# Kernel optimization log

Measured on AMD Instinct MI355X. Metric: run time of the kernel, lower is better.

Reference implementation:

```python
import jax, jax.numpy as jnp
import numpy as np

EPS = 1e-5
KS = 3  # deformable kernel size
K2 = KS * KS


def conv2d(x, w, stride=1, padding=1):
    return jax.lax.conv_general_dilated(
        x, w, window_strides=(stride, stride),
        padding=[(padding, padding), (padding, padding)],
        dimension_numbers=("NCHW", "OIHW", "NCHW"))


def batchnorm(x, gamma, beta):
    # training-mode BN: batch statistics over (N, H, W)
    mean = jnp.mean(x, axis=(0, 2, 3), keepdims=True)
    var = jnp.var(x, axis=(0, 2, 3), keepdims=True)
    xhat = (x - mean) * jax.lax.rsqrt(var + EPS)
    return xhat * gamma[None, :, None, None] + beta[None, :, None, None]


def deform_conv(x, offsets, w, pad=1):
    # x: (B,C,H,W); offsets: (B,2*K2,H,W) -> first K2 channels = row (y)
    # offsets, next K2 = col (x) offsets; w: (O,C,KS,KS)
    B, C, H, W = x.shape
    xp = jnp.pad(x, ((0, 0), (0, 0), (pad, pad), (pad, pad)))
    Hp, Wp = H + 2 * pad, W + 2 * pad
    # base grid (center of each output pixel in padded coords)
    p0_y = jnp.arange(H, dtype=x.dtype) + pad            # (H,)
    p0_x = jnp.arange(W, dtype=x.dtype) + pad            # (W,)
    # kernel tap offsets in [-1, 0, 1]^2, row-major
    pn = jnp.stack(jnp.meshgrid(jnp.arange(KS) - pad, jnp.arange(KS) - pad,
                                indexing="ij"), axis=-1).reshape(K2, 2).astype(x.dtype)
    off = offsets.reshape(B, 2, K2, H, W)
    off_y = jnp.transpose(off[:, 0], (0, 2, 3, 1))       # (B,H,W,K2)
    off_x = jnp.transpose(off[:, 1], (0, 2, 3, 1))
    py = p0_y[None, :, None, None] + pn[:, 0][None, None, None, :] + off_y
    px = p0_x[None, None, :, None] + pn[:, 1][None, None, None, :] + off_x
    py = jnp.clip(py, 0.0, Hp - 1.0)
    px = jnp.clip(px, 0.0, Wp - 1.0)
    y0 = jnp.floor(py).astype(jnp.int32)
    x0 = jnp.floor(px).astype(jnp.int32)
    y1 = jnp.minimum(y0 + 1, Hp - 1)
    x1 = jnp.minimum(x0 + 1, Wp - 1)
    wy = (py - y0.astype(x.dtype))[:, None]              # (B,1,H,W,K2)
    wx = (px - x0.astype(x.dtype))[:, None]

    def gather(xb, yi, xi):                              # xb (C,Hp,Wp)
        return xb[:, yi, xi]                             # (C,H,W,K2)
    g = jax.vmap(gather)
    v00 = g(xp, y0, x0)
    v01 = g(xp, y0, x1)
    v10 = g(xp, y1, x0)
    v11 = g(xp, y1, x1)
    sampled = (v00 * (1 - wy) * (1 - wx) + v01 * (1 - wy) * wx +
               v10 * wy * (1 - wx) + v11 * wy * wx)      # (B,C,H,W,K2)
    return jnp.einsum("bchwk,ock->bohw", sampled, w.reshape(w.shape[0], C, K2))


def setup_inputs() -> dict:
    key = jax.random.key(0)
    ks = jax.random.split(key, 16)
    B, Cin, P, H, W = 64, 64, 64, 64, 64
    s = lambda k, shp, fan: jax.random.normal(k, shp, jnp.float32) * (fan ** -0.5)
    return {
        "x": jax.random.normal(ks[0], (B, Cin, H, W), jnp.float32),
        "conv1_w": s(ks[1], (P, Cin, 3, 3), Cin * 9),
        "bn1_g": jnp.ones((P,), jnp.float32), "bn1_b": jnp.zeros((P,), jnp.float32),
        "conv2_w": s(ks[2], (16, P, 1, 1), P),
        "bn2_g": jnp.ones((16,), jnp.float32), "bn2_b": jnp.zeros((16,), jnp.float32),
        "off_w": s(ks[3], (18, 16, 3, 3), 16 * 9) * 0.1,
        "off_b": jnp.zeros((18,), jnp.float32),
        "conv3_w": s(ks[4], (16, 16, 3, 3), 16 * 9),
        "bn3_g": jnp.ones((16,), jnp.float32), "bn3_b": jnp.zeros((16,), jnp.float32),
        "conv4_w": s(ks[5], (P, 16, 3, 3), 16 * 9),
        "bn4_g": jnp.ones((P,), jnp.float32), "bn4_b": jnp.zeros((P,), jnp.float32),
    }


def reference(x, conv1_w, bn1_g, bn1_b, conv2_w, bn2_g, bn2_b, off_w, off_b,
              conv3_w, bn3_g, bn3_b, conv4_w, bn4_g, bn4_b):
    out = jax.nn.relu(batchnorm(conv2d(x, conv1_w, 1, 1), bn1_g, bn1_b))
    out = jax.nn.relu(batchnorm(conv2d(out, conv2_w, 1, 0), bn2_g, bn2_b))
    offsets = conv2d(out, off_w, 1, 1) + off_b[None, :, None, None]
    out = jax.nn.relu(batchnorm(deform_conv(out, offsets, conv3_w), bn3_g, bn3_b))
    out = batchnorm(conv2d(out, conv4_w, 1, 1), bn4_g, bn4_b)
    out = out + x  # identity shortcut (stride=1, in_planes==planes)
    return jax.nn.relu(out)
```

## Files before the change

kernel.cpp:

```cpp
#include <hip/hip_runtime.h>

#define BN_N 262144.0f

typedef unsigned short u16;
typedef __attribute__((ext_vector_type(8))) short short8;
typedef __attribute__((ext_vector_type(4))) float floatx4;

#define RP1 4224
#define IS1 278784
#define RP2 1584
#define IS2 104544
#define H2P_TOTAL 6690816

static __device__ __forceinline__ u16 f2bf(float f) {
  union { float f; unsigned u; } v; v.f = f;
  unsigned u = v.u;
  return (u16)((u + 0x7FFFu + ((u >> 16) & 1u)) >> 16);
}
static __device__ __forceinline__ float bf2f(u16 h) {
  union { unsigned u; float f; } v; v.u = ((unsigned)h) << 16;
  return v.f;
}
static __device__ __forceinline__ void cp16(const u16* g, u16* l) {
  __builtin_amdgcn_global_load_lds((const __attribute__((address_space(1))) unsigned int*)g,
                                   (__attribute__((address_space(3))) unsigned int*)l, 16, 0, 0);
}

__global__ __launch_bounds__(256) void prep_weights_k(const float* __restrict__ w1,
                                                      const float* __restrict__ w4,
                                                      const float* __restrict__ w3,
                                                      const float* __restrict__ ow,
                                                      u16* __restrict__ Bsw, u16* __restrict__ Bsw4,
                                                      u16* __restrict__ Bsw3, u16* __restrict__ BswO) {
  int blk = blockIdx.x, tid = threadIdx.x;
  if (blk < 144) {
    int d = blk * 256 + tid;
    int kin = d & 7, n = (d >> 3) & 63, kgrp = (d >> 9) & 3, kc = d >> 11;
    int k = kc * 32 + kgrp * 8 + kin;
    int tap = k >> 6, c = k & 63;
    Bsw[d] = f2bf(w1[n * 576 + c * 9 + tap]);
  } else if (blk < 184) {
    int d = (blk - 144) * 256 + tid;
    int kin = d & 7, n = (d >> 3) & 63, lkk = (d >> 9) & 3, kk = d >> 11;
    int tap = kk * 2 + (lkk >> 1);
    int c = ((lkk & 1) << 3) + kin;
    float v = (tap < 9) ? w4[n * 144 + c * 9 + tap] : 0.f;
    Bsw4[d] = f2bf(v);
  } else if (blk < 194) {
    int d = (blk - 184) * 256 + tid;
    int kin = d & 7, n = (d >> 3) & 15, lkk = (d >> 7) & 3, kk = d >> 9;
    int k = kk * 32 + lkk * 8 + kin;
    int tap = k >> 4, c = k & 15;
    float v = (tap < 9) ? w3[n * 144 + c * 9 + tap] : 0.f;
    Bsw3[d] = f2bf(v);
  } else {
    int d = (blk - 194) * 256 + tid;
    int kin = d & 7, n = (d >> 3) & 31, lkk = (d >> 8) & 3, kk = d >> 10;
    int tap = kk * 2 + (lkk >> 1);
    int c = ((lkk & 1) << 3) + kin;
    float v = (tap < 9 && n < 18) ? ow[n * 144 + c * 9 + tap] : 0.f;
    BswO[d] = f2bf(v);
  }
}

__global__ __launch_bounds__(256) void prep_x_k(const float* __restrict__ x,
                                                u16* __restrict__ xp) {
  int yp = blockIdx.x;
  int b = blockIdx.y;
  int tid = threadIdx.x;
  u16* rowbase = xp + (size_t)(b * 66 + yp) * RP1;
  if (yp == 0 || yp == 65) {
    for (int i = tid; i < RP1 / 4; i += 256)
      ((ushort4*)rowbase)[i] = make_ushort4(0, 0, 0, 0);
    return;
  }
  int y = yp - 1;
  __shared__ __align__(16) u16 s[64][72];
  for (int i = tid; i < 4096; i += 256) {
    int c = i >> 6, xx = i & 63;
    s[xx][c] = f2bf(x[((b * 64 + c) << 12) + (y << 6) + xx]);
  }
  if (tid < 128) {
    int c = tid & 63;
    int pxp = (tid >> 6) ? 65 : 0;
    rowbase[pxp * 64 + c] = 0;
  }
  __syncthreads();
  for (int j = tid; j < 512; j += 256) {
    int xx = j >> 3, chunk = j & 7;
    int pxp = xx + 1;
    int ph = chunk ^ (pxp & 7);
    *(short8*)(rowbase + pxp * 64 + ph * 8) = *(const short8*)(&s[xx][chunk * 8]);
  }
}

__global__ __launch_bounds__(512, 2) void conv1_mfma(const u16* __restrict__ xp,
                                                     const u16* __restrict__ Bsw,
                                                     u16* __restrict__ h1,
                                                     float* __restrict__ sum1, float* __restrict__ sq1) {
  __shared__ __align__(16) u16 ring[43520];
  __shared__ float LS[256], LQ[256];
  const int tid = threadIdx.x;
  const int w8 = tid >> 6, l = tid & 63;
  const int r = w8 & 3, g = w8 >> 2;
  const int lm = l & 15, lk = l >> 4;
  const int b = blockIdx.x >> 2;
  const int quarter = blockIdx.x & 3;
  const int c0 = quarter * 8;
  const u16* xb = xp + (size_t)b * 66 * RP1;

  short8 bReg[18][2];
#pragma unroll
  for (int kk = 0; kk < 18; ++kk)
#pragma unroll
    for (int j = 0; j < 2; ++j)
      bReg[kk][j] = *(const short8*)(Bsw + (((kk * 4 + lk) * 64) + (g * 2 + j) * 16 + lm) * 8);

#pragma unroll
  for (int c = 0; c < 3; ++c) {
    const u16* src = xb + (size_t)(2 * (c0 + c)) * RP1;
    u16* dst = ring + ((c0 + c) % 5) * 8704;
    for (int s = w8; s < 17; s += 8) cp16(src + s * 512 + l * 8, dst + s * 512);
  }
  asm volatile("s_waitcnt vmcnt(0)" ::: "memory");
  __builtin_amdgcn_s_barrier();
  __builtin_amdgcn_sched_barrier(0);

  float ssum[2] = {0.f, 0.f}, sqsm[2] = {0.f, 0.f};

#pragma unroll 1
  for (int j = 0; j < 4; ++j) {
    const int y0 = quarter * 16 + j * 4;
    if (j < 3) {
#pragma unroll
      for (int c = 0; c < 2; ++c) {
        const int ch = c0 + 2 * j + 3 + c;
        const u16* src = xb + (size_t)(2 * ch) * RP1;
        u16* dst = ring + (ch % 5) * 8704;
        for (int s = w8; s < 17; s += 8) cp16(src + s * 512 + l * 8, dst + s * 512);
      }
      __builtin_amdgcn_sched_barrier(0);
    }

    floatx4 acc[4][2];
#pragma unroll
    for (int mt = 0; mt < 4; ++mt)
#pragma unroll
      for (int nb = 0; nb < 2; ++nb)
        acc[mt][nb] = (floatx4){0.f, 0.f, 0.f, 0.f};

#pragma unroll
    for (int kk = 0; kk < 18; ++kk) {
      const int tap = kk >> 1;
      const int dy = (tap < 3) ? 0 : ((tap < 6) ? 1 : 2);
      const int dx = tap - dy * 3;
      const int chunk16 = ((kk & 1) << 2) + lk;
      const int pr = y0 + r + dy;
      const u16* abase = ring + ((pr >> 1) % 5) * 8704 + (pr & 1) * 4224;
      short8 aF[4];
#pragma unroll
      for (int mt = 0; mt < 4; ++mt) {
        int pxp = mt * 16 + lm + dx;
        int ph = chunk16 ^ (pxp & 7);
        aF[mt] = *(const short8*)(abase + pxp * 64 + ph * 8);
      }
#pragma unroll
      for (int mt = 0; mt < 4; ++mt)
#pragma unroll
        for (int nb = 0; nb < 2; ++nb)
          acc[mt][nb] = __builtin_amdgcn_mfma_f32_16x16x32_bf16(aF[mt], bReg[kk][nb], acc[mt][nb], 0, 0, 0);
    }

    const int y = y0 + r;
#pragma unroll
    for (int mt = 0; mt < 4; ++mt)
#pragma unroll
      for (int nb = 0; nb < 2; ++nb) {
        const int oc = g * 32 + nb * 16 + lm;
        u16* dst = h1 + ((size_t)(b * 64 + oc) << 12) + (y << 6) + mt * 16 + (lk << 2);
        floatx4 v = acc[mt][nb];
        *(ushort4*)dst = make_ushort4(f2bf(v.x), f2bf(v.y), f2bf(v.z), f2bf(v.w));
      }

#pragma unroll
    for (int nb = 0; nb < 2; ++nb)
#pragma unroll
      for (int mt = 0; mt < 4; ++mt) {
        floatx4 a = acc[mt][nb];
        ssum[nb] += a.x + a.y + a.z + a.w;
        sqsm[nb] += a.x * a.x + a.y * a.y + a.z * a.z + a.w * a.w;
      }

    if (j < 3) {
      asm volatile("s_waitcnt vmcnt(8)" ::: "memory");
      __builtin_amdgcn_s_barrier();
      __builtin_amdgcn_sched_barrier(0);
    }
  }

#pragma unroll
  for (int nb = 0; nb < 2; ++nb) {
    ssum[nb] += __shfl_xor(ssum[nb], 16, 64);  ssum[nb] += __shfl_xor(ssum[nb], 32, 64);
    sqsm[nb] += __shfl_xor(sqsm[nb], 16, 64);  sqsm[nb] += __shfl_xor(sqsm[nb], 32, 64);
  }
  if (lk == 0) {
#pragma unroll
    for (int nb = 0; nb < 2; ++nb) {
      const int oc = g * 32 + nb * 16 + lm;
      LS[r * 64 + oc] = ssum[nb];  LQ[r * 64 + oc] = sqsm[nb];
    }
  }
  __syncthreads();
  if (tid < 64) atomicAdd(&sum1[tid], LS[tid] + LS[64 + tid] + LS[128 + tid] + LS[192 + tid]);
  else if (tid < 128) { int o = tid - 64; atomicAdd(&sq1[o], LQ[o] + LQ[64 + o] + LQ[128 + o] + LQ[192 + o]); }
}

__global__ __launch_bounds__(256) void conv2_k(const u16* __restrict__ h1,
                                               const float* __restrict__ w2,
                                               const float* __restrict__ sum1, const float* __restrict__ sq1,
                                               const float* __restrict__ g1, const float* __restrict__ b1,
                                               u16* __restrict__ out,
                                               float* __restrict__ sum2, float* __restrict__ sq2) {
  __shared__ float s_wt[64 * 16];
  __shared__ float s_scale[64], s_shift[64];
  __shared__ float ls[4][16], lsq[4][16];
  int tid = threadIdx.x;
  for (int i = tid; i < 1024; i += 256) {
    int o = i >> 6, c = i & 63;
    s_wt[c * 16 + o] = w2[i];
  }
  if (tid < 64) {
    float m = sum1[tid] / BN_N;
    float var = sq1[tid] / BN_N - m * m;
    float sc = g1[tid] * rsqrtf(var + 1e-5f);
    s_scale[tid] = sc;
    s_shift[tid] = b1[tid] - m * sc;
  }
  __syncthreads();
  int p = blockIdx.x * 256 + tid;
  int b = p >> 12, r = p & 4095;
  const u16* src = h1 + ((size_t)b << 18) + r;
  float acc[16];
#pragma unroll
  for (int o = 0; o < 16; ++o) acc[o] = 0.f;
  for (int c = 0; c < 64; ++c) {
    float v = bf2f(src[c << 12]);
    v = fmaxf(v * s_scale[c] + s_shift[c], 0.f);
    const float* wp = &s_wt[c * 16];
    float4 w0 = *(const float4*)wp;
    float4 w1 = *(const float4*)(wp + 4);
    float4 w2v = *(const float4*)(wp + 8);
    float4 w3v = *(const float4*)(wp + 12);
    acc[0] += w0.x * v;  acc[1] += w0.y * v;  acc[2] += w0.z * v;  acc[3] += w0.w * v;
    acc[4] += w1.x * v;  acc[5] += w1.y * v;  acc[6] += w1.z * v;  acc[7] += w1.w * v;
    acc[8] += w2v.x * v; acc[9] += w2v.y * v; acc[10] += w2v.z * v; acc[11] += w2v.w * v;
    acc[12] += w3v.x * v; acc[13] += w3v.y * v; acc[14] += w3v.z * v; acc[15] += w3v.w * v;
  }
  u16* dst = out + (size_t)p * 16;
  short8 o0, o1;
#pragma unroll
  for (int j = 0; j < 8; ++j) {
    o0[j] = (short)f2bf(acc[j]);
    o1[j] = (short)f2bf(acc[8 + j]);
  }
  *(short8*)(dst) = o0;
  *(short8*)(dst + 8) = o1;
  int lane = tid & 63, wv = tid >> 6;
#pragma unroll
  for (int o = 0; o < 16; ++o) {
    float s = acc[o], s2 = acc[o] * acc[o];
#pragma unroll
    for (int off = 32; off > 0; off >>= 1) {
      s += __shfl_down(s, off, 64);
      s2 += __shfl_down(s2, off, 64);
    }
    if (lane == 0) { ls[wv][o] = s; lsq[wv][o] = s2; }
  }
  __syncthreads();
  if (tid < 16) atomicAdd(&sum2[tid], ls[0][tid] + ls[1][tid] + ls[2][tid] + ls[3][tid]);
  else if (tid < 32) {
    int o = tid - 16;
    atomicAdd(&sq2[o], lsq[0][o] + lsq[1][o] + lsq[2][o] + lsq[3][o]);
  }
}

__global__ __launch_bounds__(256) void bnrelu2_k(const u16* __restrict__ ws2,
                                                 const float* __restrict__ sum2, const float* __restrict__ sq2,
                                                 const float* __restrict__ g2, const float* __restrict__ b2,
                                                 u16* __restrict__ h2p) {
  __shared__ float s_scale[16], s_shift[16];
  int tid = threadIdx.x;
  if (tid < 16) {
    float m = sum2[tid] / BN_N;
    float var = sq2[tid] / BN_N - m * m;
    float sc = g2[tid] * rsqrtf(var + 1e-5f);
    s_scale[tid] = sc;
    s_shift[tid] = b2[tid] - m * sc;
  }
  __syncthreads();
  int p = blockIdx.x * 256 + tid;
  int b = p >> 12, r = p & 4095;
  int y = r >> 6, xx = r & 63;
  const u16* src = ws2 + (size_t)p * 16;
  short8 v0 = *(const short8*)(src);
  short8 v1 = *(const short8*)(src + 8);
  u16* dst = h2p + (size_t)(b * 66 + y + 1) * RP2 + (xx + 1) * 24;
  short8 o0, o1;
#pragma unroll
  for (int j = 0; j < 8; ++j) {
    o0[j] = (short)f2bf(fmaxf(bf2f((u16)v0[j]) * s_scale[j] + s_shift[j], 0.f));
    o1[j] = (short)f2bf(fmaxf(bf2f((u16)v1[j]) * s_scale[j + 8] + s_shift[j + 8], 0.f));
  }
  *(short8*)(dst) = o0;
  *(short8*)(dst + 8) = o1;
}

__global__ __launch_bounds__(256) void offdeform_mfma(const u16* __restrict__ h2p,
                                                      const u16* __restrict__ BswO,
                                                      const float* __restrict__ ob,
                                                      const u16* __restrict__ Bsw3,
                                                      u16* __restrict__ out,
                                                      float* __restrict__ sum3, float* __restrict__ sq3) {
  __shared__ __align__(16) u16 lA[9728];
  __shared__ __align__(16) u16 lB[5120];
  __shared__ float offsT[4][64][20];
  __shared__ float ls[4][16], lsq[4][16];
  const int tid = threadIdx.x;
  const int w = tid >> 6, l = tid & 63;
  const int lm = l & 15, lk = l >> 4;
  const int b = blockIdx.x >> 4;
  const int y0 = (blockIdx.x & 15) << 2;
  const int y = y0 + w;
  const u16* src = h2p + ((size_t)b * 66 + y0) * RP2;
  for (int seg = w; seg < 19; seg += 4) cp16(src + seg * 512 + l * 8, lA + seg * 512);
  for (int seg = w; seg < 10; seg += 4) cp16(BswO + seg * 512 + l * 8, lB + seg * 512);
  __syncthreads();

  floatx4 acc[4][2];
#pragma unroll
  for (int mt = 0; mt < 4; ++mt)
#pragma unroll
    for (int nb = 0; nb < 2; ++nb)
      acc[mt][nb] = (floatx4){0.f, 0.f, 0.f, 0.f};

#pragma unroll
  for (int kk = 0; kk < 5; ++kk) {
    int tap = kk * 2 + (lk >> 1);
    if (tap > 8) tap = 8;
    const int dy = tap / 3, dx = tap - dy * 3;
    const int c0 = (lk & 1) << 3;
    const int rowoff = (w + dy) * RP2;
    short8 aF[4], bF[2];
#pragma unroll
    for (int mt = 0; mt < 4; ++mt)
      aF[mt] = *(const short8*)(lA + rowoff + (mt * 16 + lm + dx) * 24 + c0);
    const u16* bp = lB + (((kk * 4 + lk) * 32) + lm) * 8;
    bF[0] = *(const short8*)(bp);
    bF[1] = *(const short8*)(bp + 128);
#pragma unroll
    for (int mt = 0; mt < 4; ++mt)
#pragma unroll
      for (int nb = 0; nb < 2; ++nb)
        acc[mt][nb] = __builtin_amdgcn_mfma_f32_16x16x32_bf16(aF[mt], bF[nb], acc[mt][nb], 0, 0, 0);
  }

#pragma unroll
  for (int mt = 0; mt < 4; ++mt)
#pragma unroll
    for (int nb = 0; nb < 2; ++nb) {
      int oc = nb * 16 + lm;
      if (oc < 18) {
        float bias = ob[oc];
        floatx4 v = acc[mt][nb];
#pragma unroll
        for (int reg = 0; reg < 4; ++reg)
          offsT[w][mt * 16 + lk * 4 + reg][oc] = v[reg] + bias;
      }
    }
  __syncthreads();

  const u16* img = h2p + (size_t)b * IS2;
  short8 bf[5];
#pragma unroll
  for (int kk = 0; kk < 5; ++kk)
    bf[kk] = *(const short8*)(Bsw3 + (((kk * 4 + lk) * 16) + lm) * 8);

  floatx4 accd[4];
#pragma unroll
  for (int mt = 0; mt < 4; ++mt) accd[mt] = (floatx4){0.f, 0.f, 0.f, 0.f};

#pragma unroll
  for (int mt = 0; mt < 4; ++mt) {
    const int x = mt * 16 + lm;
#pragma unroll
    for (int kk = 0; kk < 5; ++kk) {
      const int k0 = kk * 32 + lk * 8;
      int tap = k0 >> 4;
      const int c0 = k0 & 15;
      if (tap > 8) tap = 8;
      const int dy = tap / 3, dx = tap - dy * 3;
      float offy = offsT[w][x][tap];
      float offx = offsT[w][x][tap + 9];
      float py = (float)(y + dy) + offy;
      float px = (float)(x + dx) + offx;
      py = fminf(fmaxf(py, 0.f), 65.f);
      px = fminf(fmaxf(px, 0.f), 65.f);
      float y0f = floorf(py), x0f = floorf(px);
      int yy0 = (int)y0f, xx0 = (int)x0f;
      int yy1 = min(yy0 + 1, 65), xx1 = min(xx0 + 1, 65);
      float wy = py - y0f, wx = px - x0f;
      float w00 = (1.f - wy) * (1.f - wx), w01 = (1.f - wy) * wx;
      float w10 = wy * (1.f - wx),         w11 = wy * wx;
      short8 v00 = *(const short8*)(img + (yy0 * 66 + xx0) * 24 + c0);
      short8 v01 = *(const short8*)(img + (yy0 * 66 + xx1) * 24 + c0);
      short8 v10 = *(const short8*)(img + (yy1 * 66 + xx0) * 24 + c0);
      short8 v11 = *(const short8*)(img + (yy1 * 66 + xx1) * 24 + c0);
      short8 a;
#pragma unroll
      for (int jj = 0; jj < 8; ++jj) {
        float s = bf2f((u16)v00[jj]) * w00 + bf2f((u16)v01[jj]) * w01
                + bf2f((u16)v10[jj]) * w10 + bf2f((u16)v11[jj]) * w11;
        a[jj] = (short)f2bf(s);
      }
      accd[mt] = __builtin_amdgcn_mfma_f32_16x16x32_bf16(a, bf[kk], accd[mt], 0, 0, 0);
    }
  }

  const int pbase = (b << 12) + (y << 6);
  float s = 0.f, s2 = 0.f;
#pragma unroll
  for (int mt = 0; mt < 4; ++mt) {
    floatx4 a = accd[mt];
    s += a.x + a.y + a.z + a.w;
    s2 += a.x * a.x + a.y * a.y + a.z * a.z + a.w * a.w;
#pragma unroll
    for (int reg = 0; reg < 4; ++reg) {
      int pp = pbase + mt * 16 + lk * 4 + reg;
      out[(size_t)pp * 16 + lm] = f2bf(a[reg]);
    }
  }
  s += __shfl_xor(s, 16, 64);  s += __shfl_xor(s, 32, 64);
  s2 += __shfl_xor(s2, 16, 64); s2 += __shfl_xor(s2, 32, 64);
  if (lk == 0) { ls[w][lm] = s; lsq[w][lm] = s2; }
  __syncthreads();
  if (tid < 16) atomicAdd(&sum3[tid], ls[0][tid] + ls[1][tid] + ls[2][tid] + ls[3][tid]);
  else if (tid < 32) {
    int o = tid - 16;
    atomicAdd(&sq3[o], lsq[0][o] + lsq[1][o] + lsq[2][o] + lsq[3][o]);
  }
}

__global__ __launch_bounds__(256) void bnrelu3_k(const u16* __restrict__ wsd,
                                                 const float* __restrict__ sum3, const float* __restrict__ sq3,
                                                 const float* __restrict__ g3, const float* __restrict__ b3,
                                                 u16* __restrict__ h3p) {
  __shared__ float s_scale[16], s_shift[16];
  int tid = threadIdx.x;
  if (tid < 16) {
    float m = sum3[tid] / BN_N;
    float var = sq3[tid] / BN_N - m * m;
    float sc = g3[tid] * rsqrtf(var + 1e-5f);
    s_scale[tid] = sc;
    s_shift[tid] = b3[tid] - m * sc;
  }
  __syncthreads();
  int p = blockIdx.x * 256 + tid;
  int b = p >> 12, r = p & 4095;
  int y = r >> 6, xx = r & 63;
  const u16* src = wsd + (size_t)p * 16;
  short8 v0 = *(const short8*)(src);
  short8 v1 = *(const short8*)(src + 8);
  u16* dst = h3p + (size_t)(b * 66 + y + 1) * RP2 + (xx + 1) * 24;
  short8 o0, o1;
#pragma unroll
  for (int j = 0; j < 8; ++j) {
    o0[j] = (short)f2bf(fmaxf(bf2f((u16)v0[j]) * s_scale[j] + s_shift[j], 0.f));
    o1[j] = (short)f2bf(fmaxf(bf2f((u16)v1[j]) * s_scale[j + 8] + s_shift[j + 8], 0.f));
  }
  *(short8*)(dst) = o0;
  *(short8*)(dst + 8) = o1;
}

__global__ __launch_bounds__(256) void conv4_mfma(const u16* __restrict__ h3p,
                                                  const u16* __restrict__ Bsw4,
                                                  u16* __restrict__ h4,
                                                  float* __restrict__ sum4, float* __restrict__ sq4) {
  __shared__ __align__(16) u16 lA[9728];
  __shared__ __align__(16) u16 lB[10240];
  const int tid = threadIdx.x;
  const int w = tid >> 6, l = tid & 63;
  const int lm = l & 15, lk = l >> 4;
  const int b = blockIdx.x >> 4;
  const int y0 = (blockIdx.x & 15) << 2;
  const int y = y0 + w;
  const u16* src = h3p + ((size_t)b * 66 + y0) * RP2;
  for (int seg = w; seg < 19; seg += 4) cp16(src + seg * 512 + l * 8, lA + seg * 512);
  for (int seg = w; seg < 20; seg += 4) cp16(Bsw4 + seg * 512 + l * 8, lB + seg * 512);
  __syncthreads();

  floatx4 acc[4][4];
#pragma unroll
  for (int mt = 0; mt < 4; ++mt)
#pragma unroll
    for (int nb = 0; nb < 4; ++nb)
      acc[mt][nb] = (floatx4){0.f, 0.f, 0.f, 0.f};

#pragma unroll
  for (int kk = 0; kk < 5; ++kk) {
    int tap = kk * 2 + (lk >> 1);
    if (tap > 8) tap = 8;
    const int dy = tap / 3, dx = tap - dy * 3;
    const int c0 = (lk & 1) << 3;
    const int rowoff = (w + dy) * RP2;
    short8 aF[4], bF[4];
#pragma unroll
    for (int mt = 0; mt < 4; ++mt)
      aF[mt] = *(const short8*)(lA + rowoff + (mt * 16 + lm + dx) * 24 + c0);
    const u16* bp = lB + (((kk * 4 + lk) * 64) + lm) * 8;
    bF[0] = *(const short8*)(bp);
    bF[1] = *(const short8*)(bp + 128);
    bF[2] = *(const short8*)(bp + 256);
    bF[3] = *(const short8*)(bp + 384);
#pragma unroll
    for (int mt = 0; mt < 4; ++mt)
#pragma unroll
      for (int nb = 0; nb < 4; ++nb)
        acc[mt][nb] = __builtin_amdgcn_mfma_f32_16x16x32_bf16(aF[mt], bF[nb], acc[mt][nb], 0, 0, 0);
  }

#pragma unroll
  for (int mt = 0; mt < 4; ++mt)
#pragma unroll
    for (int nb = 0; nb < 4; ++nb) {
      u16* dst = h4 + ((size_t)(b * 64 + nb * 16 + lm) << 12) + (y << 6) + mt * 16 + (lk << 2);
      floatx4 v = acc[mt][nb];
      *(ushort4*)dst = make_ushort4(f2bf(v.x), f2bf(v.y), f2bf(v.z), f2bf(v.w));
    }

  __syncthreads();
  float* LS = (float*)lA;
  float* LQ = LS + 256;
  float s[4], s2[4];
#pragma unroll
  for (int nb = 0; nb < 4; ++nb) {
    s[nb] = 0.f; s2[nb] = 0.f;
#pragma unroll
    for (int mt = 0; mt < 4; ++mt) {
      floatx4 a = acc[mt][nb];
      s[nb] += a.x + a.y + a.z + a.w;
      s2[nb] += a.x * a.x + a.y * a.y + a.z * a.z + a.w * a.w;
    }
    s[nb] += __shfl_xor(s[nb], 16, 64);  s[nb] += __shfl_xor(s[nb], 32, 64);
    s2[nb] += __shfl_xor(s2[nb], 16, 64); s2[nb] += __shfl_xor(s2[nb], 32, 64);
  }
  if (lk == 0) {
#pragma unroll
    for (int nb = 0; nb < 4; ++nb) { LS[w * 64 + nb * 16 + lm] = s[nb]; LQ[w * 64 + nb * 16 + lm] = s2[nb]; }
  }
  __syncthreads();
  if (tid < 64) atomicAdd(&sum4[tid], LS[tid] + LS[64 + tid] + LS[128 + tid] + LS[192 + tid]);
  else if (tid < 128) { int o = tid - 64; atomicAdd(&sq4[o], LQ[o] + LQ[64 + o] + LQ[128 + o] + LQ[192 + o]); }
}

__global__ __launch_bounds__(256) void final_k(const u16* __restrict__ h4,
                                               float* __restrict__ out,
                                               const float* __restrict__ x,
                                               const float* __restrict__ sum4, const float* __restrict__ sq4,
                                               const float* __restrict__ g4, const float* __restrict__ b4) {
  __shared__ float s_scale[64], s_shift[64];
  int tid = threadIdx.x;
  if (tid < 64) {
    float m = sum4[tid] / BN_N;
    float var = sq4[tid] / BN_N - m * m;
    float sc = g4[tid] * rsqrtf(var + 1e-5f);
    s_scale[tid] = sc;
    s_shift[tid] = b4[tid] - m * sc;
  }
  __syncthreads();
  int i = (blockIdx.x * 256 + tid) * 4;
  int c = (i >> 12) & 63;
  ushort4 q = *(const ushort4*)(h4 + i);
  float4 xv = *(const float4*)(x + i);
  float sc = s_scale[c], sh = s_shift[c];
  float4 v;
  v.x = fmaxf(bf2f(q.x) * sc + sh + xv.x, 0.f);
  v.y = fmaxf(bf2f(q.y) * sc + sh + xv.y, 0.f);
  v.z = fmaxf(bf2f(q.z) * sc + sh + xv.z, 0.f);
  v.w = fmaxf(bf2f(q.w) * sc + sh + xv.w, 0.f);
  *(float4*)(out + i) = v;
}

extern "C" void kernel_launch(void* const* d_in, const int* in_sizes, int n_in,
                              void* d_out, int out_size, void* d_ws, size_t ws_size,
                              hipStream_t stream) {
  const float* x  = (const float*)d_in[0];
  const float* w1 = (const float*)d_in[1];
  const float* g1 = (const float*)d_in[2];
  const float* b1 = (const float*)d_in[3];
  const float* w2 = (const float*)d_in[4];
  const float* g2 = (const float*)d_in[5];
  const float* b2 = (const float*)d_in[6];
  const float* ow = (const float*)d_in[7];
  const float* ob = (const float*)d_in[8];
  const float* w3 = (const float*)d_in[9];
  const float* g3 = (const float*)d_in[10];
  const float* b3 = (const float*)d_in[11];
  const float* w4 = (const float*)d_in[12];
  const float* g4 = (const float*)d_in[13];
  const float* b4 = (const float*)d_in[14];
  float* out = (float*)d_out;
  float* ws = (float*)d_ws;

  float* reg0 = ws;
  float* wsd  = reg0 + 4718592;
  float* ws2  = wsd + 4194304;
  float* h2pf = ws2 + 4194304;
  float* stats = h2pf + 4460544;
  float* sum1 = stats, *sq1 = stats + 64;
  float* sum2 = stats + 128, *sq2 = stats + 144;
  float* sum3 = stats + 160, *sq3 = stats + 176;
  float* sum4 = stats + 192, *sq4 = stats + 256;
  u16* xp   = (u16*)ws;
  u16* Bsw  = (u16*)(stats + 320);
  u16* Bsw4 = Bsw + 36864;
  u16* Bsw3 = Bsw4 + 10240;
  u16* BswO = Bsw3 + 2560;
  u16* h2p  = (u16*)h2pf;
  u16* h4   = (u16*)reg0;
  u16* h1   = (u16*)out;
  u16* ws2b = (u16*)ws2;
  u16* wsdb = (u16*)wsd;

  hipMemsetAsync(stats, 0, 320 * sizeof(float), stream);
  hipMemsetAsync(h2p, 0, (size_t)H2P_TOTAL * sizeof(u16), stream);

  prep_weights_k<<<214, 256, 0, stream>>>(w1, w4, w3, ow, Bsw, Bsw4, Bsw3, BswO);
  prep_x_k<<<dim3(66, 64), 256, 0, stream>>>(x, xp);
  conv1_mfma<<<256, 512, 0, stream>>>(xp, Bsw, h1, sum1, sq1);
  conv2_k<<<1024, 256, 0, stream>>>(h1, w2, sum1, sq1, g1, b1, ws2b, sum2, sq2);
  bnrelu2_k<<<1024, 256, 0, stream>>>(ws2b, sum2, sq2, g2, b2, h2p);
  offdeform_mfma<<<1024, 256, 0, stream>>>(h2p, BswO, ob, Bsw3, wsdb, sum3, sq3);
  bnrelu3_k<<<1024, 256, 0, stream>>>(wsdb, sum3, sq3, g3, b3, h2p );
  conv4_mfma<<<1024, 256, 0, stream>>>(h2p, Bsw4, h4, sum4, sq4);
  final_k<<<16384, 256, 0, stream>>>(h4, out, x, sum4, sq4, g4, b4);
}
```

Baseline: 308.5 us.

## Fuse BN2 and BN3 apply into producer kernels via software grid barrier

Merges conv2 with its batchnorm+ReLU kernel, and the offset/deformable conv with its batchnorm+ReLU kernel. Each kernel accumulates statistics, waits at an atomic-counter grid barrier, then applies the normalization directly from register accumulators into the padded buffer. This removes two launches and the bf16 intermediate write/read round trips. It relies on all 1024 blocks being co-resident (launch_bounds occupancy hint and shared LDS aliasing), which risks deadlock and adds barrier spin overhead.

```diff
diff --git a/kernel.cpp b/kernel.cpp
--- a/kernel.cpp
+++ b/kernel.cpp
@@ -25,6 +25,16 @@
   __builtin_amdgcn_global_load_lds((const __attribute__((address_space(1))) unsigned int*)g,
                                    (__attribute__((address_space(3))) unsigned int*)l, 16, 0, 0);
 }
+static __device__ __forceinline__ void grid_barrier(unsigned* cnt, unsigned n) {
+  __syncthreads();
+  if (threadIdx.x == 0) {
+    __threadfence();
+    atomicAdd(cnt, 1u);
+    while (atomicAdd(cnt, 0u) < n) __builtin_amdgcn_s_sleep(8);
+  }
+  __syncthreads();
+}
+static __device__ __forceinline__ float atomic_read(float* p) { return atomicAdd(p, 0.f); }
 
 __global__ __launch_bounds__(256) void prep_weights_k(const float* __restrict__ w1,
                                                       const float* __restrict__ w4,
@@ -215,12 +225,13 @@
   else if (tid < 128) { int o = tid - 64; atomicAdd(&sq1[o], LQ[o] + LQ[64 + o] + LQ[128 + o] + LQ[192 + o]); }
 }
 
-__global__ __launch_bounds__(256) void conv2_k(const u16* __restrict__ h1,
-                                               const float* __restrict__ w2,
-                                               const float* __restrict__ sum1, const float* __restrict__ sq1,
-                                               const float* __restrict__ g1, const float* __restrict__ b1,
-                                               u16* __restrict__ out,
-                                               float* __restrict__ sum2, float* __restrict__ sq2) {
+__global__ __launch_bounds__(256, 4) void conv2bn_k(const u16* __restrict__ h1,
+                                                    const float* __restrict__ w2,
+                                                    const float* __restrict__ sum1, const float* __restrict__ sq1,
+                                                    const float* __restrict__ g1, const float* __restrict__ b1,
+                                                    const float* __restrict__ g2, const float* __restrict__ b2,
+                                                    float* sum2, float* sq2, unsigned* cnt2,
+                                                    u16* __restrict__ h2p) {
   __shared__ float s_wt[64 * 16];
   __shared__ float s_scale[64], s_shift[64];
   __shared__ float ls[4][16], lsq[4][16];
@@ -256,15 +267,6 @@
     acc[8] += w2v.x * v; acc[9] += w2v.y * v; acc[10] += w2v.z * v; acc[11] += w2v.w * v;
     acc[12] += w3v.x * v; acc[13] += w3v.y * v; acc[14] += w3v.z * v; acc[15] += w3v.w * v;
   }
-  u16* dst = out + (size_t)p * 16;
-  short8 o0, o1;
-#pragma unroll
-  for (int j = 0; j < 8; ++j) {
-    o0[j] = (short)f2bf(acc[j]);
-    o1[j] = (short)f2bf(acc[8 + j]);
-  }
-  *(short8*)(dst) = o0;
-  *(short8*)(dst + 8) = o1;
   int lane = tid & 63, wv = tid >> 6;
 #pragma unroll
   for (int o = 0; o < 16; ++o) {
@@ -282,49 +284,42 @@
     int o = tid - 16;
     atomicAdd(&sq2[o], lsq[0][o] + lsq[1][o] + lsq[2][o] + lsq[3][o]);
   }
-}
-
-__global__ __launch_bounds__(256) void bnrelu2_k(const u16* __restrict__ ws2,
-                                                 const float* __restrict__ sum2, const float* __restrict__ sq2,
-                                                 const float* __restrict__ g2, const float* __restrict__ b2,
-                                                 u16* __restrict__ h2p) {
-  __shared__ float s_scale[16], s_shift[16];
-  int tid = threadIdx.x;
+
+  grid_barrier(cnt2, 1024u);
+
   if (tid < 16) {
-    float m = sum2[tid] / BN_N;
-    float var = sq2[tid] / BN_N - m * m;
+    float m = atomic_read(&sum2[tid]) / BN_N;
+    float var = atomic_read(&sq2[tid]) / BN_N - m * m;
     float sc = g2[tid] * rsqrtf(var + 1e-5f);
     s_scale[tid] = sc;
     s_shift[tid] = b2[tid] - m * sc;
   }
   __syncthreads();
-  int p = blockIdx.x * 256 + tid;
-  int b = p >> 12, r = p & 4095;
   int y = r >> 6, xx = r & 63;
-  const u16* src = ws2 + (size_t)p * 16;
-  short8 v0 = *(const short8*)(src);
-  short8 v1 = *(const short8*)(src + 8);
   u16* dst = h2p + (size_t)(b * 66 + y + 1) * RP2 + (xx + 1) * 24;
   short8 o0, o1;
 #pragma unroll
   for (int j = 0; j < 8; ++j) {
-    o0[j] = (short)f2bf(fmaxf(bf2f((u16)v0[j]) * s_scale[j] + s_shift[j], 0.f));
-    o1[j] = (short)f2bf(fmaxf(bf2f((u16)v1[j]) * s_scale[j + 8] + s_shift[j + 8], 0.f));
+    o0[j] = (short)f2bf(fmaxf(acc[j] * s_scale[j] + s_shift[j], 0.f));
+    o1[j] = (short)f2bf(fmaxf(acc[8 + j] * s_scale[j + 8] + s_shift[j + 8], 0.f));
   }
   *(short8*)(dst) = o0;
   *(short8*)(dst + 8) = o1;
 }
 
-__global__ __launch_bounds__(256) void offdeform_mfma(const u16* __restrict__ h2p,
-                                                      const u16* __restrict__ BswO,
-                                                      const float* __restrict__ ob,
-                                                      const u16* __restrict__ Bsw3,
-                                                      u16* __restrict__ out,
-                                                      float* __restrict__ sum3, float* __restrict__ sq3) {
-  __shared__ __align__(16) u16 lA[9728];
-  __shared__ __align__(16) u16 lB[5120];
-  __shared__ float offsT[4][64][20];
+__global__ __launch_bounds__(256, 4) void offdeform3_k(const u16* __restrict__ h2p,
+                                                       const u16* __restrict__ BswO,
+                                                       const float* __restrict__ ob,
+                                                       const u16* __restrict__ Bsw3,
+                                                       const float* __restrict__ g3, const float* __restrict__ b3,
+                                                       float* sum3, float* sq3, unsigned* cnt3,
+                                                       u16* __restrict__ h3p) {
+  __shared__ __align__(16) u16 lmem[14848];
   __shared__ float ls[4][16], lsq[4][16];
+  __shared__ float s_scale[16], s_shift[16];
+  u16* lA = lmem;
+  u16* lB = lmem + 9728;
+  float* offsT = (float*)lmem;
   const int tid = threadIdx.x;
   const int w = tid >> 6, l = tid & 63;
   const int lm = l & 15, lk = l >> 4;
@@ -363,6 +358,7 @@
       for (int nb = 0; nb < 2; ++nb)
         acc[mt][nb] = __builtin_amdgcn_mfma_f32_16x16x32_bf16(aF[mt], bF[nb], acc[mt][nb], 0, 0, 0);
   }
+  __syncthreads();
 
 #pragma unroll
   for (int mt = 0; mt < 4; ++mt)
@@ -374,7 +370,7 @@
         floatx4 v = acc[mt][nb];
 #pragma unroll
         for (int reg = 0; reg < 4; ++reg)
-          offsT[w][mt * 16 + lk * 4 + reg][oc] = v[reg] + bias;
+          offsT[(w * 64 + mt * 16 + lk * 4 + reg) * 20 + oc] = v[reg] + bias;
       }
     }
   __syncthreads();
@@ -399,8 +395,8 @@
       const int c0 = k0 & 15;
       if (tap > 8) tap = 8;
       const int dy = tap / 3, dx = tap - dy * 3;
-      float offy = offsT[w][x][tap];
-      float offx = offsT[w][x][tap + 9];
+      float offy = offsT[(w * 64 + x) * 20 + tap];
+      float offx = offsT[(w * 64 + x) * 20 + tap + 9];
       float py = (float)(y + dy) + offy;
       float px = (float)(x + dx) + offx;
       py = fminf(fmaxf(py, 0.f), 65.f);
@@ -426,18 +422,12 @@
     }
   }
 
-  const int pbase = (b << 12) + (y << 6);
   float s = 0.f, s2 = 0.f;
 #pragma unroll
   for (int mt = 0; mt < 4; ++mt) {
     floatx4 a = accd[mt];
     s += a.x + a.y + a.z + a.w;
     s2 += a.x * a.x + a.y * a.y + a.z * a.z + a.w * a.w;
-#pragma unroll
-    for (int reg = 0; reg < 4; ++reg) {
-      int pp = pbase + mt * 16 + lk * 4 + reg;
-      out[(size_t)pp * 16 + lm] = f2bf(a[reg]);
-    }
   }
   s += __shfl_xor(s, 16, 64);  s += __shfl_xor(s, 32, 64);
   s2 += __shfl_xor(s2, 16, 64); s2 += __shfl_xor(s2, 32, 64);
@@ -448,37 +438,28 @@
     int o = tid - 16;
     atomicAdd(&sq3[o], lsq[0][o] + lsq[1][o] + lsq[2][o] + lsq[3][o]);
   }
-}
-
-__global__ __launch_bounds__(256) void bnrelu3_k(const u16* __restrict__ wsd,
-                                                 const float* __restrict__ sum3, const float* __restrict__ sq3,
-                                                 const float* __restrict__ g3, const float* __restrict__ b3,
-                                                 u16* __restrict__ h3p) {
-  __shared__ float s_scale[16], s_shift[16];
-  int tid = threadIdx.x;
+
+  grid_barrier(cnt3, 1024u);
+
   if (tid < 16) {
-    float m = sum3[tid] / BN_N;
-    float var = sq3[tid] / BN_N - m * m;
+    float m = atomic_read(&sum3[tid]) / BN_N;
+    float var = atomic_read(&sq3[tid]) / BN_N - m * m;
     float sc = g3[tid] * rsqrtf(var + 1e-5f);
     s_scale[tid] = sc;
     s_shift[tid] = b3[tid] - m * sc;
   }
   __syncthreads();
-  int p = blockIdx.x * 256 + tid;
-  int b = p >> 12, r = p & 4095;
-  int y = r >> 6, xx = r & 63;
-  const u16* src = wsd + (size_t)p * 16;
-  short8 v0 = *(const short8*)(src);
-  short8 v1 = *(const short8*)(src + 8);
-  u16* dst = h3p + (size_t)(b * 66 + y + 1) * RP2 + (xx + 1) * 24;
-  short8 o0, o1;
-#pragma unroll
-  for (int j = 0; j < 8; ++j) {
-    o0[j] = (short)f2bf(fmaxf(bf2f((u16)v0[j]) * s_scale[j] + s_shift[j], 0.f));
-    o1[j] = (short)f2bf(fmaxf(bf2f((u16)v1[j]) * s_scale[j + 8] + s_shift[j + 8], 0.f));
-  }
-  *(short8*)(dst) = o0;
-  *(short8*)(dst + 8) = o1;
+  const float sc = s_scale[lm], sh = s_shift[lm];
+  u16* rowdst = h3p + (size_t)(b * 66 + y + 1) * RP2;
+#pragma unroll
+  for (int mt = 0; mt < 4; ++mt) {
+    floatx4 a = accd[mt];
+#pragma unroll
+    for (int reg = 0; reg < 4; ++reg) {
+      int px = mt * 16 + lk * 4 + reg;
+      rowdst[(px + 1) * 24 + lm] = f2bf(fmaxf(a[reg] * sc + sh, 0.f));
+    }
+  }
 }
 
 __global__ __launch_bounds__(256) void conv4_mfma(const u16* __restrict__ h3p,
@@ -620,27 +601,25 @@
   float* sum2 = stats + 128, *sq2 = stats + 144;
   float* sum3 = stats + 160, *sq3 = stats + 176;
   float* sum4 = stats + 192, *sq4 = stats + 256;
+  unsigned* cnt2 = (unsigned*)(stats + 320);
+  unsigned* cnt3 = (unsigned*)(stats + 321);
   u16* xp   = (u16*)ws;
-  u16* Bsw  = (u16*)(stats + 320);
+  u16* Bsw  = (u16*)(stats + 384);
   u16* Bsw4 = Bsw + 36864;
   u16* Bsw3 = Bsw4 + 10240;
   u16* BswO = Bsw3 + 2560;
   u16* h2p  = (u16*)h2pf;
   u16* h4   = (u16*)reg0;
   u16* h1   = (u16*)out;
-  u16* ws2b = (u16*)ws2;
-  u16* wsdb = (u16*)wsd;
-
-  hipMemsetAsync(stats, 0, 320 * sizeof(float), stream);
+
+  hipMemsetAsync(stats, 0, 384 * sizeof(float), stream);
   hipMemsetAsync(h2p, 0, (size_t)H2P_TOTAL * sizeof(u16), stream);
 
   prep_weights_k<<<214, 256, 0, stream>>>(w1, w4, w3, ow, Bsw, Bsw4, Bsw3, BswO);
   prep_x_k<<<dim3(66, 64), 256, 0, stream>>>(x, xp);
   conv1_mfma<<<256, 512, 0, stream>>>(xp, Bsw, h1, sum1, sq1);
-  conv2_k<<<1024, 256, 0, stream>>>(h1, w2, sum1, sq1, g1, b1, ws2b, sum2, sq2);
-  bnrelu2_k<<<1024, 256, 0, stream>>>(ws2b, sum2, sq2, g2, b2, h2p);
-  offdeform_mfma<<<1024, 256, 0, stream>>>(h2p, BswO, ob, Bsw3, wsdb, sum3, sq3);
-  bnrelu3_k<<<1024, 256, 0, stream>>>(wsdb, sum3, sq3, g3, b3, h2p );
+  conv2bn_k<<<1024, 256, 0, stream>>>(h1, w2, sum1, sq1, g1, b1, g2, b2, sum2, sq2, cnt2, h2p);
+  offdeform3_k<<<1024, 256, 0, stream>>>(h2p, BswO, ob, Bsw3, g3, b3, sum3, sq3, cnt3, h2p );
   conv4_mfma<<<1024, 256, 0, stream>>>(h2p, Bsw4, h4, sum4, sq4);
   final_k<<<16384, 256, 0, stream>>>(h4, out, x, sum4, sq4, g4, b4);
 }
```

New measurement: 476.1 us. 1.54x slower.
